# Kernel tuning notes

Measured on AMD Instinct MI355X. Metric: run time of the kernel, lower is better.

## Reference

```python
import jax, jax.numpy as jnp
import numpy as np

H = 512
W = 512
N_STROKES = 5000
S = 10          # samples_per_curve
K = 20          # strokes_per_pixel
CANVAS_COLOR = 0.5  # 'gray'
COARSE = 5      # coarse grid downsample factor (H//5, W//5)


def setup_inputs() -> dict:
    key = jax.random.key(0)
    ks = jax.random.split(key, 6)
    # stroke centers spread over the canvas
    location = jax.random.uniform(ks[0], (N_STROKES, 2), jnp.float32) * jnp.array([H, W], jnp.float32)
    # bezier control-point offsets relative to the stroke center
    curve_s = jax.random.normal(ks[1], (N_STROKES, 2), jnp.float32) * 8.0
    curve_e = jax.random.normal(ks[2], (N_STROKES, 2), jnp.float32) * 8.0
    curve_c = jax.random.normal(ks[3], (N_STROKES, 2), jnp.float32) * 8.0
    color = jax.random.uniform(ks[4], (N_STROKES, 3), jnp.float32)
    width = jax.random.uniform(ks[5], (N_STROKES, 1), jnp.float32) * 4.0 + 1.0
    return {"curve_s": curve_s, "curve_e": curve_e, "curve_c": curve_c,
            "color": color, "location": location, "width": width}


def _bezier_points(s, c, e, num_points):
    # s, c, e: [N, 2] -> [N, num_points, 2]
    t = jnp.linspace(0.0, 1.0, num_points).astype(jnp.float32)  # [S]
    omt2 = (1.0 - t) ** 2  # [S]
    t2 = t ** 2
    # x/y computed identically: c + (1-t)^2 (s - c) + t^2 (e - c)
    pts = c[:, None, :] + omt2[None, :, None] * (s - c)[:, None, :] \
          + t2[None, :, None] * (e - c)[:, None, :]
    return pts  # [N, S, 2]


def _nearest_upsample_idx(out_size, in_size):
    # torch F.interpolate mode='nearest': src = floor(dst * in/out)
    idx = jnp.floor(jnp.arange(out_size) * (in_size / out_size)).astype(jnp.int32)
    return jnp.clip(idx, 0, in_size - 1)


def reference(curve_s, curve_e, curve_c, color, location, width):
    # sample bezier curve points (absolute coords)
    pts = _bezier_points(curve_s + location, curve_c + location,
                         curve_e + location, S)  # [N, S, 2]

    # ---- coarse-grid KNN over stroke centers ----
    Hc, Wc = H // COARSE, W // COARSE
    tH = jnp.linspace(0.0, float(H), Hc).astype(jnp.float32)
    tW = jnp.linspace(0.0, float(W), Wc).astype(jnp.float32)
    Px, Py = jnp.meshgrid(tH, tW, indexing='ij')
    P = jnp.stack([Px, Py], axis=-1)  # [Hc, Wc, 2]
    D_centers = jnp.sum(jnp.square(P[:, :, None, :] - location), axis=-1)  # [Hc, Wc, N]
    _, idcs = jax.lax.top_k(-D_centers, K)  # [Hc, Wc, K]

    near_pts = pts[idcs]      # [Hc, Wc, K, S, 2]
    near_col = color[idcs]    # [Hc, Wc, K, 3]
    near_w = width[idcs]      # [Hc, Wc, K, 1]

    # ---- upsample coarse gathers to full res ----
    ih = _nearest_upsample_idx(H, Hc)
    iw = _nearest_upsample_idx(W, Wc)
    near_pts = near_pts[ih][:, iw]   # [H, W, K, S, 2] (nearest)
    near_col = near_col[ih][:, iw]   # [H, W, K, 3]   (nearest)
    # widths: bilinear (align_corners=False, no antialias) per channel
    near_w = jax.image.resize(near_w[..., 0], (H, W, K), method='linear')[..., None]  # [H, W, K, 1]

    # ---- full-res pixel grid ----
    tHf = jnp.linspace(0.0, float(H), H).astype(jnp.float32)
    tWf = jnp.linspace(0.0, float(W), W).astype(jnp.float32)
    Pxf, Pyf = jnp.meshgrid(tHf, tWf, indexing='ij')
    P_full = jnp.stack([Pxf, Pyf], axis=-1)  # [H, W, 2]

    # ---- per-pixel closest point on each polyline segment ----
    a = near_pts[:, :, :, :S - 1, :]              # [H, W, K, S-1, 2]
    b_a = near_pts[:, :, :, 1:, :] - a            # segment direction
    pa = P_full[:, :, None, None, :] - a          # pixel - segment start
    t = jnp.sum(b_a * pa, axis=-1) / jnp.sum(jnp.square(b_a), axis=-1)
    t = jnp.clip(t, 0.0, 1.0)
    closest = a + t[..., None] * b_a
    dist = jnp.sum(jnp.square(P_full[:, :, None, None, :] - closest), axis=-1)  # [H, W, K, S-1]

    D = jnp.min(dist, axis=(-1, -2))  # [H, W]
    min_per_stroke = jnp.min(dist, axis=-1)  # [H, W, K]
    ranking = jax.nn.softmax(100000.0 * (1.0 / (1e-08 + min_per_stroke)), axis=-1)  # [H, W, K]

    I_colors = jnp.einsum('hwkf,hwk->hwf', near_col, ranking)  # [H, W, 3]
    bs = jnp.einsum('hwkf,hwk->hwf', near_w, ranking)          # [H, W, 1]
    bs_mask = jax.nn.sigmoid(bs - D[..., None])
    canvas = jnp.full_like(I_colors, CANVAS_COLOR)
    I = I_colors * bs_mask + (1.0 - bs_mask) * canvas
    return I
```

## Files before the change

kernel.cpp:

```cpp
#include <hip/hip_runtime.h>
#include <math.h>

#define NS 5000
#define SS 10
#define KK 20
#define HC 102
#define NBIN 32
#define BINW 16.0f
#define NPB 20
#define CAP 192

#define WAVE_SYNC() __asm__ volatile("s_waitcnt lgkmcnt(0)" ::: "memory")

__global__ void __launch_bounds__(256) prep_kernel(
        const float* __restrict__ cs, const float* __restrict__ ce,
        const float* __restrict__ cc, const float* __restrict__ loc,
        const float* __restrict__ color, const float* __restrict__ width,
        float* __restrict__ sdata, float4* __restrict__ ctab,
        int* __restrict__ binCntP) {
    __shared__ int4 lcnt4[NBIN*NBIN/4];
    int* lcnt = (int*)lcnt4;
    int t = threadIdx.x;
    lcnt4[t] = make_int4(0, 0, 0, 0);
    __syncthreads();
    int i = blockIdx.x * 256 + t;
    if (i < NS) {
        float lx = loc[i*2+0], ly = loc[i*2+1];
        float sx = cs[i*2+0] + lx, sy = cs[i*2+1] + ly;
        float ex = ce[i*2+0] + lx, ey = ce[i*2+1] + ly;
        float px = cc[i*2+0] + lx, py = cc[i*2+1] + ly;
        float qx[SS], qy[SS];
        #pragma unroll
        for (int j = 0; j < SS; ++j) {
            float tt = (float)j * (1.0f / 9.0f);
            float omt = 1.0f - tt;
            float omt2 = omt * omt, t2 = tt * tt;
            qx[j] = px + omt2 * (sx - px) + t2 * (ex - px);
            qy[j] = py + omt2 * (sy - py) + t2 * (ey - py);
            sdata[i*32 + 2*j + 0] = qx[j];
            sdata[i*32 + 2*j + 1] = qy[j];
        }
        #pragma unroll
        for (int sg = 0; sg < 9; ++sg) {
            float bx = qx[sg+1] - qx[sg], by = qy[sg+1] - qy[sg];
            sdata[i*32 + 20 + sg] = 1.0f / (bx*bx + by*by);
        }
        sdata[i*32 + 29] = 0.0f; sdata[i*32 + 30] = 0.0f; sdata[i*32 + 31] = 0.0f;
        ctab[i] = make_float4(color[i*3+0], color[i*3+1], color[i*3+2], width[i]);
        int b0 = min(max((int)(lx * (1.0f/BINW)), 0), NBIN-1);
        int b1 = min(max((int)(ly * (1.0f/BINW)), 0), NBIN-1);
        atomicAdd(&lcnt[b0*NBIN + b1], 1);
    }
    __syncthreads();
    ((int4*)binCntP)[blockIdx.x * 256 + t] = lcnt4[t];
}

__global__ void __launch_bounds__(256) scatter_kernel(
        const float* __restrict__ loc, const int* __restrict__ binCntP,
        int* __restrict__ binStart, float2* __restrict__ sxy, int* __restrict__ sid) {
    __shared__ int fill[NBIN*NBIN];
    __shared__ int wsum[4];
    int t = threadIdx.x, lane = t & 63, w = t >> 6;
    int mb = blockIdx.x;
    int4 tot = make_int4(0,0,0,0), bel = make_int4(0,0,0,0);
    for (int b = 0; b < NPB; ++b) {
        int4 v = ((const int4*)binCntP)[b * 256 + t];
        tot.x += v.x; tot.y += v.y; tot.z += v.z; tot.w += v.w;
        if (b < mb) { bel.x += v.x; bel.y += v.y; bel.z += v.z; bel.w += v.w; }
    }
    int s0 = tot.x, s1 = s0 + tot.y, s2 = s1 + tot.z, s3 = s2 + tot.w;
    int x = s3;
    #pragma unroll
    for (int off = 1; off < 64; off <<= 1) {
        int y = __shfl_up(x, off, 64);
        if (lane >= off) x += y;
    }
    if (lane == 63) wsum[w] = x;
    __syncthreads();
    int woff = 0;
    #pragma unroll
    for (int i = 0; i < 4; ++i) woff += (i < w) ? wsum[i] : 0;
    int texcl = woff + x - s3;
    fill[4*t+0] = texcl      + bel.x;
    fill[4*t+1] = texcl + s0 + bel.y;
    fill[4*t+2] = texcl + s1 + bel.z;
    fill[4*t+3] = texcl + s2 + bel.w;
    if (mb == 0) {
        binStart[4*t+1] = texcl + s0;
        binStart[4*t+2] = texcl + s1;
        binStart[4*t+3] = texcl + s2;
        binStart[4*t+4] = texcl + s3;
        if (t == 0) binStart[0] = 0;
    }
    __syncthreads();
    int i = mb * 256 + t;
    if (i < NS) {
        float l0 = loc[i*2+0], l1 = loc[i*2+1];
        int b0 = min(max((int)(l0 * (1.0f/BINW)), 0), NBIN-1);
        int b1 = min(max((int)(l1 * (1.0f/BINW)), 0), NBIN-1);
        int pos = atomicAdd(&fill[b0*NBIN + b1], 1);
        sxy[pos] = make_float2(l0, l1);
        sid[pos] = i;
    }
}

__global__ void __launch_bounds__(256) topk_kernel(const float* __restrict__ loc,
                                                   const float* __restrict__ width,
                                                   const float2* __restrict__ sxy,
                                                   const int* __restrict__ sid,
                                                   const int* __restrict__ binStart,
                                                   int* __restrict__ idcs,
                                                   float* __restrict__ wk) {
    __shared__ unsigned long long sk[4][CAP];
    int w = threadIdx.x >> 6, lane = threadIdx.x & 63;
    int cell = blockIdx.x * 4 + w;
    int ci = cell / HC, cj = cell - ci * HC;
    const float dc = 512.0f / 101.0f;
    float c0 = (float)ci * dc;
    float c1 = (float)cj * dc;
    unsigned long long below = (1ull << lane) - 1ull;

    float R = 30.0f;
    int cnt = 0;
    for (int attempt = 0; attempt < 5; ++attempt) {
        float R2 = R * R;
        int base = 0;
        int by0 = max((int)((c0 - R) * (1.0f/BINW)), 0);
        int by1 = min((int)((c0 + R) * (1.0f/BINW)), NBIN-1);
        int bx0 = max((int)((c1 - R) * (1.0f/BINW)), 0);
        int bx1 = min((int)((c1 + R) * (1.0f/BINW)), NBIN-1);
        for (int by = by0; by <= by1; ++by) {
            int s = binStart[by*NBIN + bx0];
            int e = binStart[by*NBIN + bx1 + 1];
            for (int t0 = s; t0 < e; t0 += 64) {
                int t = t0 + lane;
                int tc = min(t, e - 1);
                float2 p = sxy[tc];
                float dx = c0 - p.x, dy = c1 - p.y;
                float d = dx*dx + dy*dy;
                bool pred = (t < e) && (d < R2);
                unsigned long long mask = __ballot(pred);
                int pos = base + __popcll(mask & below);
                if (pred && pos < CAP)
                    sk[w][pos] = ((unsigned long long)__float_as_uint(d) << 32)
                               | (unsigned int)sid[tc];
                base += __popcll(mask);
            }
        }
        cnt = base;
        if (cnt >= KK) break;
        R *= 1.6f;
    }
    WAVE_SYNC();

    if (cnt >= KK && cnt <= CAP) {
        if (cnt <= 64) {
            unsigned long long k0 = (lane < cnt) ? sk[w][lane] : ~0ull;
            int r0 = 0;
            int j = 0;
            #pragma unroll 1
            for (; j + 4 <= cnt; j += 4) {
                unsigned long long a = sk[w][j],   b = sk[w][j+1];
                unsigned long long c = sk[w][j+2], d = sk[w][j+3];
                r0 += (int)(a < k0) + (int)(b < k0) + (int)(c < k0) + (int)(d < k0);
            }
            for (; j < cnt; ++j) r0 += (int)(sk[w][j] < k0);
            if (r0 < KK && lane < cnt) {
                int idx = (int)(unsigned int)(k0 & 0xffffffffull);
                idcs[cell*KK + r0] = idx;
                wk[cell*KK + r0]   = width[idx];
            }
        } else {
            unsigned long long k0 = (lane       < cnt) ? sk[w][lane]       : ~0ull;
            unsigned long long k1 = (lane + 64  < cnt) ? sk[w][lane + 64]  : ~0ull;
            unsigned long long k2 = (lane + 128 < cnt) ? sk[w][lane + 128] : ~0ull;
            int r0 = 0, r1 = 0, r2 = 0;
            #pragma unroll 1
            for (int j = 0; j < cnt; ++j) {
                unsigned long long a = sk[w][j];
                r0 += (int)(a < k0); r1 += (int)(a < k1); r2 += (int)(a < k2);
            }
            if (r0 < KK && lane < cnt) {
                int idx = (int)(unsigned int)(k0 & 0xffffffffull);
                idcs[cell*KK + r0] = idx;  wk[cell*KK + r0] = width[idx];
            }
            if (r1 < KK && lane + 64 < cnt) {
                int idx = (int)(unsigned int)(k1 & 0xffffffffull);
                idcs[cell*KK + r1] = idx;  wk[cell*KK + r1] = width[idx];
            }
            if (r2 < KK && lane + 128 < cnt) {
                int idx = (int)(unsigned int)(k2 & 0xffffffffull);
                idcs[cell*KK + r2] = idx;  wk[cell*KK + r2] = width[idx];
            }
        }
    } else {
        if (lane == 0) {
            float bd[KK]; int bi[KK];
            for (int k = 0; k < KK; ++k) { bd[k] = 3.4e38f; bi[k] = 0; }
            for (int n = 0; n < NS; ++n) {
                float dx = c0 - loc[n*2+0];
                float dy = c1 - loc[n*2+1];
                float d = dx*dx + dy*dy;
                if (d < bd[KK-1]) {
                    int p = KK - 1;
                    while (p > 0 && bd[p-1] > d) { bd[p] = bd[p-1]; bi[p] = bi[p-1]; --p; }
                    bd[p] = d; bi[p] = n;
                }
            }
            for (int k = 0; k < KK; ++k) {
                idcs[cell*KK + k] = bi[k];
                wk[cell*KK + k]   = width[bi[k]];
            }
        }
    }
}

__global__ void __launch_bounds__(256, 4) render_kernel(const float* __restrict__ sdata,
                                                        const float4* __restrict__ ctab,
                                                        const int* __restrict__ idcs,
                                                        const float* __restrict__ wk,
                                                        float* __restrict__ out) {
    int tt0 = threadIdx.x, lane = tt0 & 63, wq = tt0 >> 6;
    int x = blockIdx.x * 16 + ((wq & 1) << 3) + (lane & 7);
    int y = blockIdx.y * 16 + ((wq >> 1) << 3) + (lane >> 3);
    const float df = 512.0f / 511.0f;
    float p0 = (float)y * df;
    float p1 = (float)x * df;
    int cy = (y * 51) >> 8;
    int cx = (x * 51) >> 8;

    const int4* mip = (const int4*)(idcs + (cy * HC + cx) * KK);
    int4 m0 = mip[0], m1 = mip[1], m2 = mip[2], m3 = mip[3], m4 = mip[4];
    int idxs[KK] = {m0.x,m0.y,m0.z,m0.w, m1.x,m1.y,m1.z,m1.w, m2.x,m2.y,m2.z,m2.w,
                    m3.x,m3.y,m3.z,m3.w, m4.x,m4.y,m4.z,m4.w};

    const float sc = 102.0f / 512.0f;
    float iny = ((float)y + 0.5f) * sc - 0.5f;
    float inx = ((float)x + 0.5f) * sc - 0.5f;
    float y0f = floorf(iny), x0f = floorf(inx);
    float fy = iny - y0f, fx = inx - x0f;
    int y0 = min(max((int)y0f, 0), HC - 1);
    int y1 = min(max((int)y0f + 1, 0), HC - 1);
    int x0 = min(max((int)x0f, 0), HC - 1);
    int x1 = min(max((int)x0f + 1, 0), HC - 1);
    const float* w00 = wk + (y0 * HC + x0) * KK;
    const float* w01 = wk + (y0 * HC + x1) * KK;
    const float* w10 = wk + (y1 * HC + x0) * KK;
    const float* w11 = wk + (y1 * HC + x1) * KK;

    float m = -INFINITY, s = 0.0f;
    float a0 = 0.0f, a1 = 0.0f, a2 = 0.0f, wa = 0.0f;
    float D = INFINITY;

    #pragma unroll 4
    for (int k = 0; k < KK; ++k) {
        const float4* sp = (const float4*)(sdata + idxs[k] * 32);
        float4 f0 = sp[0], f1 = sp[1], f2 = sp[2], f3 = sp[3], f4 = sp[4];
        float4 i0 = sp[5], i1 = sp[6], i2 = sp[7];
        float4 cw = ctab[idxs[k]];
        float qx[10] = {f0.x, f0.z, f1.x, f1.z, f2.x, f2.z, f3.x, f3.z, f4.x, f4.z};
        float qy[10] = {f0.y, f0.w, f1.y, f1.w, f2.y, f2.w, f3.y, f3.w, f4.y, f4.w};
        float iv[9]  = {i0.x, i0.y, i0.z, i0.w, i1.x, i1.y, i1.z, i1.w, i2.x};
        float mink = INFINITY;
        #pragma unroll
        for (int sg = 0; sg < 9; ++sg) {
            float ax = qx[sg], ay = qy[sg];
            float bx = qx[sg+1] - ax, by = qy[sg+1] - ay;
            float pax = p0 - ax, pay = p1 - ay;
            float dot = bx * pax + by * pay;
            float tt = dot * iv[sg];
            tt = fminf(fmaxf(tt, 0.0f), 1.0f);
            float ccx = ax + tt * bx, ccy = ay + tt * by;
            float ddx = p0 - ccx, ddy = p1 - ccy;
            float d = ddx * ddx + ddy * ddy;
            mink = fminf(mink, d);
        }
        D = fminf(D, mink);
        float z = 100000.0f / (1e-8f + mink);
        float wkv = (1.0f - fy) * ((1.0f - fx) * w00[k] + fx * w01[k])
                  +          fy * ((1.0f - fx) * w10[k] + fx * w11[k]);
        float nm  = fmaxf(m, z);
        float scl = __expf(m - nm);
        float e   = __expf(z - nm);
        s  = s  * scl + e;
        a0 = a0 * scl + cw.x * e;
        a1 = a1 * scl + cw.y * e;
        a2 = a2 * scl + cw.z * e;
        wa = wa * scl + wkv  * e;
        m = nm;
    }
    float inv = 1.0f / s;
    float bs = wa * inv;
    float msk = 1.0f / (1.0f + __expf(-(bs - D)));
    float o0 = a0 * inv * msk + (1.0f - msk) * 0.5f;
    float o1 = a1 * inv * msk + (1.0f - msk) * 0.5f;
    float o2 = a2 * inv * msk + (1.0f - msk) * 0.5f;
    int base = (y * 512 + x) * 3;
    out[base+0] = o0;
    out[base+1] = o1;
    out[base+2] = o2;
}

extern "C" void kernel_launch(void* const* d_in, const int* in_sizes, int n_in,
                              void* d_out, int out_size, void* d_ws, size_t ws_size,
                              hipStream_t stream) {
    const float* cs    = (const float*)d_in[0];
    const float* ce    = (const float*)d_in[1];
    const float* cc    = (const float*)d_in[2];
    const float* color = (const float*)d_in[3];
    const float* loc   = (const float*)d_in[4];
    const float* width = (const float*)d_in[5];
    float* out = (float*)d_out;

    char* p = (char*)d_ws;
    float*  sdata    = (float*)p;                 p += NS * 32 * sizeof(float);
    float4* ctab     = (float4*)p;                p += NS * sizeof(float4);
    int*    idcs     = (int*)p;                   p += (size_t)HC*HC*KK*sizeof(int);
    float*  wk       = (float*)p;                 p += (size_t)HC*HC*KK*sizeof(float);
    int*    binCntP  = (int*)p;                   p += NPB * NBIN*NBIN * sizeof(int);
    int*    binStart = (int*)p;                   p += 4112;
    float2* sxy      = (float2*)p;                p += NS * sizeof(float2);
    int*    sid      = (int*)p;

    prep_kernel   <<<NPB, 256, 0, stream>>>(cs, ce, cc, loc, color, width, sdata, ctab, binCntP);
    scatter_kernel<<<NPB, 256, 0, stream>>>(loc, binCntP, binStart, sxy, sid);
    topk_kernel   <<<(HC*HC)/4, 256, 0, stream>>>(loc, width, sxy, sid, binStart, idcs, wk);
    render_kernel <<<dim3(32, 32), 256, 0, stream>>>(sdata, ctab, idcs, wk, out);
}
```

Baseline: 131.6 us.

## Split the 20 neighbor strokes across two waves per pixel and merge softmax via LDS

The render kernel now uses 512 threads per block, so each pixel is handled by two waves that each process 10 of the 20 candidate strokes. The second wave writes its partial online-softmax state (max, sum, weighted color and width accumulators, min distance) to shared memory. The first wave merges the two states and writes the output. This doubles thread-level parallelism and shortens each thread's dependent loop, at the cost of a block barrier, LDS traffic and idle lanes in the final merge.

New measurement: 157.8 us. +20.0%, slower.

```diff
diff --git a/kernel.cpp b/kernel.cpp
--- a/kernel.cpp
+++ b/kernel.cpp
@@ -215,24 +215,22 @@
     }
 }
 
-__global__ void __launch_bounds__(256, 4) render_kernel(const float* __restrict__ sdata,
+__global__ void __launch_bounds__(512, 8) render_kernel(const float* __restrict__ sdata,
                                                         const float4* __restrict__ ctab,
                                                         const int* __restrict__ idcs,
                                                         const float* __restrict__ wk,
                                                         float* __restrict__ out) {
-    int tt0 = threadIdx.x, lane = tt0 & 63, wq = tt0 >> 6;
-    int x = blockIdx.x * 16 + ((wq & 1) << 3) + (lane & 7);
-    int y = blockIdx.y * 16 + ((wq >> 1) << 3) + (lane >> 3);
+    __shared__ float part[4][7][64];
+    int tid = threadIdx.x, lane = tid & 63, wv = tid >> 6;
+    int h = wv & 1, q = wv >> 1;
+    int x = blockIdx.x * 16 + ((q & 1) << 3) + (lane & 7);
+    int y = blockIdx.y * 16 + ((q >> 1) << 3) + (lane >> 3);
     const float df = 512.0f / 511.0f;
     float p0 = (float)y * df;
     float p1 = (float)x * df;
     int cy = (y * 51) >> 8;
     int cx = (x * 51) >> 8;
-
-    const int4* mip = (const int4*)(idcs + (cy * HC + cx) * KK);
-    int4 m0 = mip[0], m1 = mip[1], m2 = mip[2], m3 = mip[3], m4 = mip[4];
-    int idxs[KK] = {m0.x,m0.y,m0.z,m0.w, m1.x,m1.y,m1.z,m1.w, m2.x,m2.y,m2.z,m2.w,
-                    m3.x,m3.y,m3.z,m3.w, m4.x,m4.y,m4.z,m4.w};
+    const int* mi = idcs + (cy * HC + cx) * KK;
 
     const float sc = 102.0f / 512.0f;
     float iny = ((float)y + 0.5f) * sc - 0.5f;
@@ -252,12 +250,15 @@
     float a0 = 0.0f, a1 = 0.0f, a2 = 0.0f, wa = 0.0f;
     float D = INFINITY;
 
+    int kbeg = h * 10;
     #pragma unroll 4
-    for (int k = 0; k < KK; ++k) {
-        const float4* sp = (const float4*)(sdata + idxs[k] * 32);
+    for (int kk = 0; kk < 10; ++kk) {
+        int k = kbeg + kk;
+        int idx = mi[k];
+        const float4* sp = (const float4*)(sdata + idx * 32);
         float4 f0 = sp[0], f1 = sp[1], f2 = sp[2], f3 = sp[3], f4 = sp[4];
         float4 i0 = sp[5], i1 = sp[6], i2 = sp[7];
-        float4 cw = ctab[idxs[k]];
+        float4 cw = ctab[idx];
         float qx[10] = {f0.x, f0.z, f1.x, f1.z, f2.x, f2.z, f3.x, f3.z, f4.x, f4.z};
         float qy[10] = {f0.y, f0.w, f1.y, f1.w, f2.y, f2.w, f3.y, f3.w, f4.y, f4.w};
         float iv[9]  = {i0.x, i0.y, i0.z, i0.w, i1.x, i1.y, i1.z, i1.w, i2.x};
@@ -289,16 +290,37 @@
         wa = wa * scl + wkv  * e;
         m = nm;
     }
-    float inv = 1.0f / s;
-    float bs = wa * inv;
-    float msk = 1.0f / (1.0f + __expf(-(bs - D)));
-    float o0 = a0 * inv * msk + (1.0f - msk) * 0.5f;
-    float o1 = a1 * inv * msk + (1.0f - msk) * 0.5f;
-    float o2 = a2 * inv * msk + (1.0f - msk) * 0.5f;
-    int base = (y * 512 + x) * 3;
-    out[base+0] = o0;
-    out[base+1] = o1;
-    out[base+2] = o2;
+
+    if (h == 1) {
+        part[q][0][lane] = m;  part[q][1][lane] = s;  part[q][2][lane] = a0;
+        part[q][3][lane] = a1; part[q][4][lane] = a2; part[q][5][lane] = wa;
+        part[q][6][lane] = D;
+    }
+    __syncthreads();
+    if (h == 0) {
+        float mB  = part[q][0][lane], sB  = part[q][1][lane], a0B = part[q][2][lane];
+        float a1B = part[q][3][lane], a2B = part[q][4][lane], waB = part[q][5][lane];
+        float DB  = part[q][6][lane];
+        float nm = fmaxf(m, mB);
+        float eA = __expf(m - nm), eB = __expf(mB - nm);
+        s  = s  * eA + sB  * eB;
+        a0 = a0 * eA + a0B * eB;
+        a1 = a1 * eA + a1B * eB;
+        a2 = a2 * eA + a2B * eB;
+        wa = wa * eA + waB * eB;
+        D = fminf(D, DB);
+
+        float inv = 1.0f / s;
+        float bs = wa * inv;
+        float msk = 1.0f / (1.0f + __expf(-(bs - D)));
+        float o0 = a0 * inv * msk + (1.0f - msk) * 0.5f;
+        float o1 = a1 * inv * msk + (1.0f - msk) * 0.5f;
+        float o2 = a2 * inv * msk + (1.0f - msk) * 0.5f;
+        int base = (y * 512 + x) * 3;
+        out[base+0] = o0;
+        out[base+1] = o1;
+        out[base+2] = o2;
+    }
 }
 
 extern "C" void kernel_launch(void* const* d_in, const int* in_sizes, int n_in,
@@ -325,5 +347,5 @@
     prep_kernel   <<<NPB, 256, 0, stream>>>(cs, ce, cc, loc, color, width, sdata, ctab, binCntP);
     scatter_kernel<<<NPB, 256, 0, stream>>>(loc, binCntP, binStart, sxy, sid);
     topk_kernel   <<<(HC*HC)/4, 256, 0, stream>>>(loc, width, sxy, sid, binStart, idcs, wk);
-    render_kernel <<<dim3(32, 32), 256, 0, stream>>>(sdata, ctab, idcs, wk, out);
-}
+    render_kernel <<<dim3(32, 32), 512, 0, stream>>>(sdata, ctab, idcs, wk, out);
+}
```
